# Optimization experiments

Hardware: AMD Instinct MI355X
Metric: run time of the kernel (lower is better)

## Reference

```python
import jax, jax.numpy as jnp
import numpy as np

BLOCK = 128          # fp8 quantization block size (from linear_deepseek_v3)
FP8_MAX = 448.0      # max representable value of float8_e4m3fn
F8 = jnp.float8_e4m3fn
G, T, K, N = 8, 1024, 7168, 2048


def setup_inputs() -> dict:
    key = jax.random.key(0)
    kx, kw, kb = jax.random.split(key, 3)
    xs = jax.random.normal(kx, (G, T, K), jnp.float32)
    # Build an fp8 block-quantized weight + per-(128x128)-block fp32 scale,
    # matching the stored self.weight (fp8) and self.scale parameters.
    w_raw = jax.random.normal(kw, (G, N, K), jnp.float32)
    wb = w_raw.reshape(G, N // BLOCK, BLOCK, K // BLOCK, BLOCK)
    amax = jnp.max(jnp.abs(wb), axis=(2, 4))            # [G, NB, KB]
    scale = amax / FP8_MAX
    w_q = (wb / scale[:, :, None, :, None]).astype(F8).astype(jnp.float32)
    weight = w_q.reshape(G, N, K)                        # fp8 code values held in fp32
    bias = jax.random.normal(kb, (G, N), jnp.float32) * 0.02
    return {"xs": xs, "weight": weight, "scale": scale, "bias": bias}


def reference(xs, weight, scale, bias):
    """Grouped fp8 block-quantized GEMM with inline dequant.
    xs:     [G, T, K] fp32 activations (one slab per group)
    weight: [G, N, K] fp8-quantized weights (stored as fp32 code values)
    scale:  [G, N/128, K/128] fp32 per-block weight scales
    bias:   [G, N] fp32
    """
    g, t, k = xs.shape
    n = weight.shape[1]
    kb, nb = k // BLOCK, n // BLOCK
    # --- act_quant_deepseek_v3: per (token, 128-col block) absmax/448 scale ---
    xb = xs.reshape(g, t, kb, BLOCK)
    a_scale = jnp.max(jnp.abs(xb), axis=-1) / FP8_MAX        # [G, T, KB]
    x_q = (xb / a_scale[..., None]).astype(F8).astype(jnp.float32)
    x_deq = (x_q * a_scale[..., None]).reshape(g, t, k)      # fused dequant
    # --- weight dequant: broadcast per-(128x128)-block scale ---
    w_deq = (weight.reshape(g, nb, BLOCK, kb, BLOCK)
             * scale[:, :, None, :, None]).reshape(g, n, k)
    # --- grouped GEMM (y = x A^T) + bias, fp32 accumulation ---
    y = jnp.einsum('gtk,gnk->gtn', x_deq, w_deq) + bias[:, None, :]
    return y
```

## Files before the change

kernel.cpp:

```cpp
#include <hip/hip_runtime.h>
#include <hip/hip_bf16.h>
#include <stdint.h>

#define G_ 8
#define T_ 1024
#define K_ 7168
#define N_ 2048
#define KB_ 56
#define NB_ 16
#define NT8_ 56

typedef __attribute__((ext_vector_type(4))) float f32x4;
typedef __attribute__((ext_vector_type(8))) int   i32x8;

typedef __attribute__((address_space(3))) uint32_t lds_u32_t;
typedef const __attribute__((address_space(1))) uint32_t gbl_u32_t;

__device__ __forceinline__ void gload_lds16(const void* gsrc, const void* ldst)
{
    __builtin_amdgcn_global_load_lds(
        (gbl_u32_t*)(uintptr_t)gsrc,
        (lds_u32_t*)(uint32_t)(uintptr_t)ldst, 16, 0, 0);
}

__device__ __forceinline__ void blockbar()
{
    asm volatile("" ::: "memory");
    __builtin_amdgcn_s_barrier();
    asm volatile("" ::: "memory");
}

__global__ __launch_bounds__(256) void act_quant_kernel(
    const float* __restrict__ xs, uint8_t* __restrict__ xq8,
    float* __restrict__ ascale)
{
    const int grp = (blockIdx.x * 256 + threadIdx.x) >> 5;
    const int l   = threadIdx.x & 31;
    const size_t base = (size_t)grp * 128 + (size_t)l * 4;

    const float4 v = *(const float4*)(xs + base);
    float am = fmaxf(fmaxf(fabsf(v.x), fabsf(v.y)),
                     fmaxf(fabsf(v.z), fabsf(v.w)));
#pragma unroll
    for (int off = 1; off <= 16; off <<= 1)
        am = fmaxf(am, __shfl_xor(am, off, 64));

    const float rs = 448.0f / am;
    const float s  = am * (1.0f / 448.0f);

    int pk = __builtin_amdgcn_cvt_pk_fp8_f32(v.x * rs, v.y * rs, 0, false);
    pk     = __builtin_amdgcn_cvt_pk_fp8_f32(v.z * rs, v.w * rs, pk, true);
    *(uint32_t*)(xq8 + base) = (uint32_t)pk;

    if (l == 0) {
        const int kb = grp % KB_;
        const int t  = (grp / KB_) & (T_ - 1);
        const int g  = grp / (KB_ * T_);
        ascale[(((size_t)(g * 4 + (t >> 8))) * KB_ + kb) * 256 + (t & 255)] = s;
    }
}

union Frag { i32x8 v; struct { int4 lo, hi; } p; };

#define RD_FRAG(dst, base, r)                                                 \
  { const int rx_ = ((r) & 7) << 4;                                           \
    const char* bp_ = smem + (base) + (r)*128;                                \
    dst.p.lo = *(const int4*)(bp_ + ((lhi*32) ^ rx_));                        \
    dst.p.hi = *(const int4*)(bp_ + ((lhi*32 + 16) ^ rx_)); }

#define STG_A(c, t, bb) gload_lds16(pA8[c] + (size_t)(t)*128,                 \
      smem + (bb)*16384 + (c)*4096 + tid*16)
#define STG_S(c) gload_lds16(pS + (size_t)(c)*2048,                           \
      smem + 65536 + ((c)&1)*4096 + tid*16)

#define LOAD_B(t)                                                             \
  { _Pragma("unroll") for (int i = 0; i < 16; ++i)                            \
      br[i] = *(const f32x4*)(pWb + (size_t)(t)*128 + (size_t)i*(2*K_)); }

#define CVT_WRITE_B(bb)                                                       \
  { _Pragma("unroll") for (int i = 0; i < 16; ++i) {                          \
      int pk_ = __builtin_amdgcn_cvt_pk_fp8_f32(br[i][0], br[i][1], 0, false);\
      pk_ = __builtin_amdgcn_cvt_pk_fp8_f32(br[i][2], br[i][3], pk_, true);   \
      const int r_ = wid*32 + i*2 + lp;                                       \
      *(uint32_t*)(smem + 32768 + (bb)*16384 + r_*128 +                       \
          (((l31 >> 2) ^ (r_ & 7)) << 4) + (l31 & 3)*4) = (uint32_t)pk_;      \
  } }

__global__ __launch_bounds__(256, 2) void gemm_fp8_kernel(
    const uint8_t* __restrict__ xq8, const float* __restrict__ w,
    const float* __restrict__ ascale, const float* __restrict__ wscale,
    const float* __restrict__ bias, float* __restrict__ y)
{
    __shared__ char smem[73984];

    const int bx0 = blockIdx.x;
    const int g     = bx0 & 7;
    const int inner = bx0 >> 3;
    const int tn    = inner >> 3;
    const int tm    = inner & 7;
    const int t0 = tm * 128, n0 = tn * 128;

    const int tid = threadIdx.x, lane = tid & 63, wid = tid >> 6;
    const int l15 = lane & 15, lhi = lane >> 4;
    const int l31 = lane & 31, lp = lane >> 5;
    const int wrow = (wid >> 1) * 64;
    const int wcol = (wid & 1) * 64;

    const uint8_t* Ag = xq8 + (size_t)g * T_ * K_;
    const float*   Wg = w   + (size_t)g * N_ * K_;

    const uint8_t* pA8[4];
#pragma unroll
    for (int c = 0; c < 4; ++c)
        pA8[c] = Ag + (size_t)(t0 + c * 32 + (tid >> 3)) * K_
                    + ((tid & 7) ^ ((tid >> 3) & 7)) * 16;

    const float* pWb = Wg + (size_t)(n0 + wid * 32 + lp) * K_ + l31 * 4;

    const float* pS = ascale + ((size_t)(g * 4 + (tm >> 1)) * KB_) * 256
                    + (tid >> 5) * 256 + (tm & 1) * 128 + (tid & 31) * 4;

    const f32x4 z4 = {0.f, 0.f, 0.f, 0.f};
    f32x4 acc[4][4] = {};
    Frag bF[4];
    f32x4 br[16];

    if (tid < KB_) {
        const float wv = wscale[((size_t)(g * NB_ + tn)) * KB_ + tid];
        *(float*)(smem + 73728 + tid * 4) = wv;
    }
    LOAD_B(0);
    asm volatile("s_waitcnt vmcnt(0)" ::: "memory");
    CVT_WRITE_B(0);
#pragma unroll
    for (int c = 0; c < 4; ++c) STG_A(c, 0, 0);
    STG_S(0);
    asm volatile("s_waitcnt vmcnt(0)" ::: "memory");
    asm volatile("s_waitcnt lgkmcnt(0)" ::: "memory");
    blockbar();

    for (int u = 0; u < NT8_; ++u) {
        const int cur = u & 1, nxt = cur ^ 1;
        const bool pf = (u + 1 < NT8_);
        const int abuf = (u >> 3) & 1;

        if ((u & 7) == 0 && u + 8 < NT8_) STG_S((u >> 3) + 1);
        if (pf) {
            LOAD_B(u + 1);
#pragma unroll
            for (int c = 0; c < 4; ++c) STG_A(c, u + 1, nxt);
        }

        const float wsc = *(const float*)(smem + 73728 + u * 4);

#pragma unroll
        for (int n = 0; n < 4; ++n)
            RD_FRAG(bF[n], 32768 + cur * 16384, wcol + n * 16 + l15);

        asm volatile("s_waitcnt lgkmcnt(0)" ::: "memory");
        __builtin_amdgcn_s_setprio(1);
#pragma unroll
        for (int m = 0; m < 4; ++m) {
            Frag aF;
            const int r = wrow + m * 16 + l15;
            RD_FRAG(aF, cur * 16384, r);
            const float4 sv = *(const float4*)(smem + 65536 + abuf * 4096 +
                (u & 7) * 512 + (wrow + m * 16 + lhi * 4) * 4);
            const float a0 = sv.x * wsc, a1 = sv.y * wsc,
                        a2 = sv.z * wsc, a3 = sv.w * wsc;
#pragma unroll
            for (int n = 0; n < 4; ++n) {
                f32x4 blk = __builtin_amdgcn_mfma_scale_f32_16x16x128_f8f6f4(
                    aF.v, bF[n].v, z4, 0, 0, 0, 0x7F7F7F7F, 0, 0x7F7F7F7F);
                acc[m][n][0] += blk[0] * a0;
                acc[m][n][1] += blk[1] * a1;
                acc[m][n][2] += blk[2] * a2;
                acc[m][n][3] += blk[3] * a3;
            }
        }
        __builtin_amdgcn_s_setprio(0);

        if (pf) {
            asm volatile("s_waitcnt vmcnt(4)" ::: "memory");
            CVT_WRITE_B(nxt);
            asm volatile("s_waitcnt vmcnt(0)" ::: "memory");
            asm volatile("s_waitcnt lgkmcnt(0)" ::: "memory");
            blockbar();
        }
    }

    float* Yg = y + (size_t)g * T_ * N_;
#pragma unroll
    for (int n = 0; n < 4; ++n) {
        const int col = n0 + wcol + n * 16 + l15;
        const float bv = bias[g * N_ + col];
#pragma unroll
        for (int m = 0; m < 4; ++m) {
            const int r0 = t0 + wrow + m * 16 + lhi * 4;
#pragma unroll
            for (int j = 0; j < 4; ++j)
                Yg[(size_t)(r0 + j) * N_ + col] = acc[m][n][j] + bv;
        }
    }
}

extern "C" void kernel_launch(void* const* d_in, const int* in_sizes, int n_in,
                              void* d_out, int out_size, void* d_ws, size_t ws_size,
                              hipStream_t stream)
{
    const float* xs     = (const float*)d_in[0];
    const float* weight = (const float*)d_in[1];
    const float* scale  = (const float*)d_in[2];
    const float* bias   = (const float*)d_in[3];
    float* y = (float*)d_out;

    uint8_t* xq8  = (uint8_t*)d_ws;
    float*   ascl = (float*)((char*)d_ws + 58720256);

    act_quant_kernel<<<(G_ * T_ * KB_) / 8, 256, 0, stream>>>(xs, xq8, ascl);
    gemm_fp8_kernel<<<G_ * (T_ / 128) * (N_ / 128), 256, 0, stream>>>(
        xq8, weight, ascl, scale, bias, y);
}
```

Measured before the change: 394.4 us.

## Pre-convert fp32 weights to fp8 in a fused prep kernel and stage via LDS DMA

```diff
diff --git a/kernel.cpp b/kernel.cpp
--- a/kernel.cpp
+++ b/kernel.cpp
@@ -10,6 +10,9 @@
 #define NB_ 16
 #define NT8_ 56
 
+#define ACT_WGS  57344
+#define WREC_WGS 28672
+
 typedef __attribute__((ext_vector_type(4))) float f32x4;
 typedef __attribute__((ext_vector_type(8))) int   i32x8;
 
@@ -30,33 +33,48 @@
     asm volatile("" ::: "memory");
 }
 
-__global__ __launch_bounds__(256) void act_quant_kernel(
+__global__ __launch_bounds__(256) void prep_kernel(
     const float* __restrict__ xs, uint8_t* __restrict__ xq8,
-    float* __restrict__ ascale)
-{
-    const int grp = (blockIdx.x * 256 + threadIdx.x) >> 5;
-    const int l   = threadIdx.x & 31;
-    const size_t base = (size_t)grp * 128 + (size_t)l * 4;
-
-    const float4 v = *(const float4*)(xs + base);
-    float am = fmaxf(fmaxf(fabsf(v.x), fabsf(v.y)),
-                     fmaxf(fabsf(v.z), fabsf(v.w)));
-#pragma unroll
-    for (int off = 1; off <= 16; off <<= 1)
-        am = fmaxf(am, __shfl_xor(am, off, 64));
-
-    const float rs = 448.0f / am;
-    const float s  = am * (1.0f / 448.0f);
-
-    int pk = __builtin_amdgcn_cvt_pk_fp8_f32(v.x * rs, v.y * rs, 0, false);
-    pk     = __builtin_amdgcn_cvt_pk_fp8_f32(v.z * rs, v.w * rs, pk, true);
-    *(uint32_t*)(xq8 + base) = (uint32_t)pk;
-
-    if (l == 0) {
-        const int kb = grp % KB_;
-        const int t  = (grp / KB_) & (T_ - 1);
-        const int g  = grp / (KB_ * T_);
-        ascale[(((size_t)(g * 4 + (t >> 8))) * KB_ + kb) * 256 + (t & 255)] = s;
+    float* __restrict__ ascale,
+    const float* __restrict__ w, uint8_t* __restrict__ wq8)
+{
+    const int bid = blockIdx.x;
+    if (bid < ACT_WGS) {
+        const int grp = (bid * 256 + threadIdx.x) >> 5;
+        const int l   = threadIdx.x & 31;
+        const size_t base = (size_t)grp * 128 + (size_t)l * 4;
+
+        const float4 v = *(const float4*)(xs + base);
+        float am = fmaxf(fmaxf(fabsf(v.x), fabsf(v.y)),
+                         fmaxf(fabsf(v.z), fabsf(v.w)));
+#pragma unroll
+        for (int off = 1; off <= 16; off <<= 1)
+            am = fmaxf(am, __shfl_xor(am, off, 64));
+
+        const float rs = 448.0f / am;
+        const float s  = am * (1.0f / 448.0f);
+
+        int pk = __builtin_amdgcn_cvt_pk_fp8_f32(v.x * rs, v.y * rs, 0, false);
+        pk     = __builtin_amdgcn_cvt_pk_fp8_f32(v.z * rs, v.w * rs, pk, true);
+        *(uint32_t*)(xq8 + base) = (uint32_t)pk;
+
+        if (l == 0) {
+            const int kb = grp % KB_;
+            const int t  = (grp / KB_) & (T_ - 1);
+            const int g  = grp / (KB_ * T_);
+            ascale[(((size_t)(g * 4 + (t >> 8))) * KB_ + kb) * 256 + (t & 255)] = s;
+        }
+    } else {
+        const size_t i = ((size_t)(bid - ACT_WGS) * 256 + threadIdx.x) * 16;
+        uint32_t o[4];
+#pragma unroll
+        for (int q = 0; q < 4; ++q) {
+            const float4 a = *(const float4*)(w + i + q * 4);
+            int pk = __builtin_amdgcn_cvt_pk_fp8_f32(a.x, a.y, 0, false);
+            pk     = __builtin_amdgcn_cvt_pk_fp8_f32(a.z, a.w, pk, true);
+            o[q] = (uint32_t)pk;
+        }
+        *(uint4*)(wq8 + i) = make_uint4(o[0], o[1], o[2], o[3]);
     }
 }
 
@@ -70,52 +88,42 @@
 
 #define STG_A(c, t, bb) gload_lds16(pA8[c] + (size_t)(t)*128,                 \
       smem + (bb)*16384 + (c)*4096 + tid*16)
+#define STG_B(c, t, bb) gload_lds16(pB8[c] + (size_t)(t)*128,                 \
+      smem + 32768 + (bb)*16384 + (c)*4096 + tid*16)
 #define STG_S(c) gload_lds16(pS + (size_t)(c)*2048,                           \
       smem + 65536 + ((c)&1)*4096 + tid*16)
 
-#define LOAD_B(t)                                                             \
-  { _Pragma("unroll") for (int i = 0; i < 16; ++i)                            \
-      br[i] = *(const f32x4*)(pWb + (size_t)(t)*128 + (size_t)i*(2*K_)); }
-
-#define CVT_WRITE_B(bb)                                                       \
-  { _Pragma("unroll") for (int i = 0; i < 16; ++i) {                          \
-      int pk_ = __builtin_amdgcn_cvt_pk_fp8_f32(br[i][0], br[i][1], 0, false);\
-      pk_ = __builtin_amdgcn_cvt_pk_fp8_f32(br[i][2], br[i][3], pk_, true);   \
-      const int r_ = wid*32 + i*2 + lp;                                       \
-      *(uint32_t*)(smem + 32768 + (bb)*16384 + r_*128 +                       \
-          (((l31 >> 2) ^ (r_ & 7)) << 4) + (l31 & 3)*4) = (uint32_t)pk_;      \
-  } }
-
 __global__ __launch_bounds__(256, 2) void gemm_fp8_kernel(
-    const uint8_t* __restrict__ xq8, const float* __restrict__ w,
+    const uint8_t* __restrict__ xq8, const uint8_t* __restrict__ wq8,
     const float* __restrict__ ascale, const float* __restrict__ wscale,
     const float* __restrict__ bias, float* __restrict__ y)
 {
-    __shared__ char smem[73984];
+    __shared__ char smem[73952];
 
     const int bx0 = blockIdx.x;
     const int g     = bx0 & 7;
     const int inner = bx0 >> 3;
-    const int tn    = inner >> 3;
-    const int tm    = inner & 7;
+    const int tn    = inner & 15;
+    const int tm    = inner >> 4;
     const int t0 = tm * 128, n0 = tn * 128;
 
     const int tid = threadIdx.x, lane = tid & 63, wid = tid >> 6;
     const int l15 = lane & 15, lhi = lane >> 4;
-    const int l31 = lane & 31, lp = lane >> 5;
     const int wrow = (wid >> 1) * 64;
     const int wcol = (wid & 1) * 64;
 
     const uint8_t* Ag = xq8 + (size_t)g * T_ * K_;
-    const float*   Wg = w   + (size_t)g * N_ * K_;
-
+    const uint8_t* Bg = wq8 + (size_t)g * N_ * K_;
+
+    const int srow = tid >> 3;
+    const int xoff = ((tid & 7) ^ (srow & 7)) * 16;
     const uint8_t* pA8[4];
-#pragma unroll
-    for (int c = 0; c < 4; ++c)
-        pA8[c] = Ag + (size_t)(t0 + c * 32 + (tid >> 3)) * K_
-                    + ((tid & 7) ^ ((tid >> 3) & 7)) * 16;
-
-    const float* pWb = Wg + (size_t)(n0 + wid * 32 + lp) * K_ + l31 * 4;
+    const uint8_t* pB8[4];
+#pragma unroll
+    for (int c = 0; c < 4; ++c) {
+        pA8[c] = Ag + (size_t)(t0 + c * 32 + srow) * K_ + xoff;
+        pB8[c] = Bg + (size_t)(n0 + c * 32 + srow) * K_ + xoff;
+    }
 
     const float* pS = ascale + ((size_t)(g * 4 + (tm >> 1)) * KB_) * 256
                     + (tid >> 5) * 256 + (tm & 1) * 128 + (tid & 31) * 4;
@@ -123,18 +131,14 @@
     const f32x4 z4 = {0.f, 0.f, 0.f, 0.f};
     f32x4 acc[4][4] = {};
     Frag bF[4];
-    f32x4 br[16];
 
     if (tid < KB_) {
         const float wv = wscale[((size_t)(g * NB_ + tn)) * KB_ + tid];
         *(float*)(smem + 73728 + tid * 4) = wv;
     }
-    LOAD_B(0);
-    asm volatile("s_waitcnt vmcnt(0)" ::: "memory");
-    CVT_WRITE_B(0);
-#pragma unroll
-    for (int c = 0; c < 4; ++c) STG_A(c, 0, 0);
     STG_S(0);
+#pragma unroll
+    for (int c = 0; c < 4; ++c) { STG_A(c, 0, 0); STG_B(c, 0, 0); }
     asm volatile("s_waitcnt vmcnt(0)" ::: "memory");
     asm volatile("s_waitcnt lgkmcnt(0)" ::: "memory");
     blockbar();
@@ -142,13 +146,12 @@
     for (int u = 0; u < NT8_; ++u) {
         const int cur = u & 1, nxt = cur ^ 1;
         const bool pf = (u + 1 < NT8_);
-        const int abuf = (u >> 3) & 1;
+        const int sbuf = (u >> 3) & 1;
 
         if ((u & 7) == 0 && u + 8 < NT8_) STG_S((u >> 3) + 1);
         if (pf) {
-            LOAD_B(u + 1);
-#pragma unroll
-            for (int c = 0; c < 4; ++c) STG_A(c, u + 1, nxt);
+#pragma unroll
+            for (int c = 0; c < 4; ++c) { STG_A(c, u + 1, nxt); STG_B(c, u + 1, nxt); }
         }
 
         const float wsc = *(const float*)(smem + 73728 + u * 4);
@@ -157,14 +160,12 @@
         for (int n = 0; n < 4; ++n)
             RD_FRAG(bF[n], 32768 + cur * 16384, wcol + n * 16 + l15);
 
-        asm volatile("s_waitcnt lgkmcnt(0)" ::: "memory");
         __builtin_amdgcn_s_setprio(1);
 #pragma unroll
         for (int m = 0; m < 4; ++m) {
             Frag aF;
-            const int r = wrow + m * 16 + l15;
-            RD_FRAG(aF, cur * 16384, r);
-            const float4 sv = *(const float4*)(smem + 65536 + abuf * 4096 +
+            RD_FRAG(aF, cur * 16384, wrow + m * 16 + l15);
+            const float4 sv = *(const float4*)(smem + 65536 + sbuf * 4096 +
                 (u & 7) * 512 + (wrow + m * 16 + lhi * 4) * 4);
             const float a0 = sv.x * wsc, a1 = sv.y * wsc,
                         a2 = sv.z * wsc, a3 = sv.w * wsc;
@@ -181,10 +182,7 @@
         __builtin_amdgcn_s_setprio(0);
 
         if (pf) {
-            asm volatile("s_waitcnt vmcnt(4)" ::: "memory");
-            CVT_WRITE_B(nxt);
             asm volatile("s_waitcnt vmcnt(0)" ::: "memory");
-            asm volatile("s_waitcnt lgkmcnt(0)" ::: "memory");
             blockbar();
         }
     }
@@ -216,8 +214,11 @@
 
     uint8_t* xq8  = (uint8_t*)d_ws;
     float*   ascl = (float*)((char*)d_ws + 58720256);
-
-    act_quant_kernel<<<(G_ * T_ * KB_) / 8, 256, 0, stream>>>(xs, xq8, ascl);
+    uint8_t* wq8  = (uint8_t*)((char*)d_ws + 60555264);
+
+    prep_kernel<<<ACT_WGS + WREC_WGS, 256, 0, stream>>>(
+        xs, xq8, ascl, weight, wq8);
+
     gemm_fp8_kernel<<<G_ * (T_ / 128) * (N_ / 128), 256, 0, stream>>>(
-        xq8, weight, ascl, scale, bias, y);
-}
+        xq8, wq8, ascl, scale, bias, y);
+}
```

New measurement: 340.2 us. -13.7%, faster.
